# Kernel optimization log

Measured on AMD Instinct MI355X. Metric: run time of the kernel, lower is better.

The kernel has to match this reference:

```python
import jax, jax.numpy as jnp
import numpy as np

B, T_ENC, H_ENC, H_DEC, ATTN = 64, 4096, 512, 512, 256


def setup_inputs() -> dict:
    key = jax.random.key(0)
    k1, k2, k3, k4, k5 = jax.random.split(key, 5)
    decoder_state = jax.random.normal(k1, (B, H_DEC), dtype=jnp.float32)
    encoder_outputs = jax.random.normal(k2, (B, T_ENC, H_ENC), dtype=jnp.float32)
    # nn.Linear(in, out, bias=False) weight has shape (out, in); apply as x @ W.T
    W_enc = jax.random.normal(k3, (ATTN, H_ENC), dtype=jnp.float32) * (1.0 / np.sqrt(H_ENC))
    W_dec = jax.random.normal(k4, (ATTN, H_DEC), dtype=jnp.float32) * (1.0 / np.sqrt(H_DEC))
    v = jax.random.normal(k5, (1, ATTN), dtype=jnp.float32) * (1.0 / np.sqrt(ATTN))
    return {"decoder_state": decoder_state, "encoder_outputs": encoder_outputs,
            "W_enc": W_enc, "W_dec": W_dec, "v": v}


def reference(decoder_state, encoder_outputs, W_enc, W_dec, v):
    # enc_proj: (B, T, A); dec_proj: (B, 1, A)
    enc_proj = jnp.einsum('bte,ae->bta', encoder_outputs, W_enc)
    dec_proj = jnp.einsum('bd,ad->ba', decoder_state, W_dec)[:, None, :]
    energy = jnp.tanh(enc_proj + dec_proj)              # (B, T, A)
    scores = jnp.einsum('bta,a->bt', energy, v[0])      # (B, T)
    attn_weights = jax.nn.softmax(scores, axis=1)       # (B, T)
    context = jnp.einsum('bte,bt->be', encoder_outputs, attn_weights)  # (B, H_enc)
    return context, attn_weights
```

## Files before the change

kernel.cpp:

```cpp
#include <hip/hip_runtime.h>
#include <hip/hip_bf16.h>

#define B 64
#define T_ENC 4096
#define H_ENC 512
#define H_DEC 512
#define ATTN 256

#define BM 128
#define BK 64
#define LDA_A 72
#define NCH_PER_B (T_ENC / BM)
#define NCHUNKS ((B * T_ENC) / BM)

typedef __attribute__((ext_vector_type(8))) short bf16x8;
typedef __attribute__((ext_vector_type(4))) float f32x4;

__device__ __forceinline__ ushort2 cvt2_bf16(float x, float y) {
    __hip_bfloat162 h = __float22bfloat162_rn(make_float2(x, y));
    return *reinterpret_cast<ushort2*>(&h);
}

__device__ __forceinline__ float fast_tanh(float x) {
    float ax = fabsf(x);
    float e = __expf(2.0f * fminf(ax, 15.0f));
    float t = 1.0f - 2.0f / (e + 1.0f);
    return copysignf(t, x);
}

__device__ __forceinline__ void gload_lds16(const void* g, void* l) {
    __builtin_amdgcn_global_load_lds(
        (const __attribute__((address_space(1))) void*)g,
        (__attribute__((address_space(3))) void*)l, 16, 0, 0);
}

__global__ void convw_kernel(const float* __restrict__ W,
                             unsigned short* __restrict__ out) {
    int g = blockIdx.x * 256 + threadIdx.x;
    int j = g & 7;
    int r = (g >> 3) & 255;
    int t = g >> 11;
    int c0 = t * 64 + ((j ^ (r & 7)) << 3);
    const float* src = W + (size_t)r * H_ENC + c0;
    float4 x0 = *(const float4*)(src);
    float4 x1 = *(const float4*)(src + 4);
    ushort2 a0 = cvt2_bf16(x0.x, x0.y);
    ushort2 a1 = cvt2_bf16(x0.z, x0.w);
    ushort2 a2 = cvt2_bf16(x1.x, x1.y);
    ushort2 a3 = cvt2_bf16(x1.z, x1.w);
    ushort4 lo = {a0.x, a0.y, a1.x, a1.y};
    ushort4 hi = {a2.x, a2.y, a3.x, a3.y};
    *(ushort4*)(out + (size_t)g * 8)     = lo;
    *(ushort4*)(out + (size_t)g * 8 + 4) = hi;
}

__global__ void decproj_kernel(const float* __restrict__ dec,
                               const float* __restrict__ Wdec,
                               float* __restrict__ dproj) {
    __shared__ float sdec[H_DEC];
    int b = blockIdx.x;
    int tid = threadIdx.x;
    sdec[tid]       = dec[b * H_DEC + tid];
    sdec[tid + 256] = dec[b * H_DEC + tid + 256];
    __syncthreads();
    const float* wrow = Wdec + (size_t)tid * H_DEC;
    float acc = 0.0f;
#pragma unroll 4
    for (int k = 0; k < H_DEC; k += 4) {
        float4 w4 = *(const float4*)(wrow + k);
        acc += w4.x * sdec[k] + w4.y * sdec[k + 1] + w4.z * sdec[k + 2] + w4.w * sdec[k + 3];
    }
    dproj[b * ATTN + tid] = acc;
}

__global__ __launch_bounds__(256, 2) void fused_kernel(
    const float* __restrict__ enc,
    const unsigned short* __restrict__ wencb,
    const float* __restrict__ dproj,
    const float* __restrict__ v,
    float* __restrict__ scores,
    float* __restrict__ ctxp,
    float* __restrict__ ml)
{
    __shared__ __align__(16) unsigned short Abuf[BM * LDA_A];
    __shared__ __align__(16) unsigned short Bbuf[ATTN * BK];
    __shared__ float sPart[BM * 2];
    __shared__ float sP[BM];
    __shared__ float sW[4];

    const int tid  = threadIdx.x;
    const int wave = tid >> 6;
    const int lane = tid & 63;
    const int quad = lane >> 4;
    const int l16  = lane & 15;
    const int wr   = wave >> 1;
    const int wc   = wave & 1;
    const int swz  = (l16 & 7) << 4;
    const int chunk = blockIdx.x;
    const int m0   = chunk * BM;
    const int b    = chunk >> 5;

    f32x4 acc[4][8];
#pragma unroll
    for (int mi = 0; mi < 4; ++mi)
#pragma unroll
        for (int ni = 0; ni < 8; ++ni) {
            f32x4 z = {0.0f, 0.0f, 0.0f, 0.0f};
            acc[mi][ni] = z;
        }

    const char* wb = (const char*)wencb;
    char* bb = (char*)Bbuf;

    for (int k0 = 0; k0 < H_ENC; k0 += BK) {
        const int t = k0 >> 6;
#pragma unroll
        for (int i = 0; i < 8; ++i) {
            int u = i * 256 + tid;
            gload_lds16(wb + (((size_t)t * 2048 + u) << 4), bb + (u << 4));
        }
#pragma unroll
        for (int rp = 0; rp < 4; ++rp) {
            int idx = rp * 2048 + tid * 8;
            int r = idx >> 6, c = idx & 63;
            const float* p = enc + (size_t)(m0 + r) * H_ENC + k0 + c;
            float4 x0 = *(const float4*)(p);
            float4 x1 = *(const float4*)(p + 4);
            ushort2 a0 = cvt2_bf16(x0.x, x0.y);
            ushort2 a1 = cvt2_bf16(x0.z, x0.w);
            ushort2 a2 = cvt2_bf16(x1.x, x1.y);
            ushort2 a3 = cvt2_bf16(x1.z, x1.w);
            union { bf16x8 v8; unsigned short u[8]; } U;
            U.u[0] = a0.x; U.u[1] = a0.y; U.u[2] = a1.x; U.u[3] = a1.y;
            U.u[4] = a2.x; U.u[5] = a2.y; U.u[6] = a3.x; U.u[7] = a3.y;
            *(bf16x8*)(&Abuf[r * LDA_A + c]) = U.v8;
        }
        __syncthreads();

#pragma unroll
        for (int kk = 0; kk < 2; ++kk) {
            bf16x8 af[4], bfv[8];
            const int ca = kk * 32 + quad * 8;
            const int dc = kk * 64 + quad * 16;
#pragma unroll
            for (int mi = 0; mi < 4; ++mi)
                af[mi] = *(const bf16x8*)(&Abuf[(wr * 64 + mi * 16 + l16) * LDA_A + ca]);
#pragma unroll
            for (int ni = 0; ni < 8; ++ni) {
                int a = wc * 128 + ni * 16 + l16;
                bfv[ni] = *(const bf16x8*)(bb + a * 128 + (dc ^ swz));
            }
#pragma unroll
            for (int mi = 0; mi < 4; ++mi)
#pragma unroll
                for (int ni = 0; ni < 8; ++ni)
                    acc[mi][ni] = __builtin_amdgcn_mfma_f32_16x16x32_bf16(
                        af[mi], bfv[ni], acc[mi][ni], 0, 0, 0);
        }
        __syncthreads();
    }

    float decp[8], vv[8];
#pragma unroll
    for (int ni = 0; ni < 8; ++ni) {
        int a = wc * 128 + ni * 16 + l16;
        decp[ni] = dproj[b * ATTN + a];
        vv[ni]   = v[a];
    }
#pragma unroll
    for (int mi = 0; mi < 4; ++mi) {
#pragma unroll
        for (int r = 0; r < 4; ++r) {
            float sum = 0.0f;
#pragma unroll
            for (int ni = 0; ni < 8; ++ni)
                sum += fast_tanh(acc[mi][ni][r] + decp[ni]) * vv[ni];
            sum += __shfl_xor(sum, 1);
            sum += __shfl_xor(sum, 2);
            sum += __shfl_xor(sum, 4);
            sum += __shfl_xor(sum, 8);
            if (l16 == 0)
                sPart[(wr * 64 + mi * 16 + quad * 4 + r) * 2 + wc] = sum;
        }
    }
    __syncthreads();

    const bool act = tid < BM;
    float s = -INFINITY;
    if (act) {
        s = sPart[tid * 2] + sPart[tid * 2 + 1];
        scores[m0 + tid] = s;
    }
    float m = s;
#pragma unroll
    for (int o = 1; o < 64; o <<= 1) m = fmaxf(m, __shfl_xor(m, o));
    if (act && lane == 0) sW[wave] = m;
    __syncthreads();
    const float M = fmaxf(sW[0], sW[1]);
    float p = act ? __expf(s - M) : 0.0f;
    float l = p;
#pragma unroll
    for (int o = 1; o < 64; o <<= 1) l += __shfl_xor(l, o);
    if (act && lane == 0) sW[2 + wave] = l;
    if (act) sP[tid] = p;
    __syncthreads();
    if (tid == 0) {
        ml[chunk * 2]     = M;
        ml[chunk * 2 + 1] = sW[2] + sW[3];
    }

    int e0 = tid * 2;
    const float* ebase = enc + (size_t)m0 * H_ENC + e0;
    float cx = 0.0f, cy = 0.0f;
#pragma unroll 8
    for (int tt = 0; tt < BM; ++tt) {
        float wt = sP[tt];
        float2 x = *(const float2*)(ebase + (size_t)tt * H_ENC);
        cx += wt * x.x;
        cy += wt * x.y;
    }
    float* cp = ctxp + (size_t)chunk * H_ENC + e0;
    cp[0] = cx;
    cp[1] = cy;
}

__global__ __launch_bounds__(256) void combine_kernel(
    const float* __restrict__ scores,
    const float* __restrict__ ctxp,
    const float* __restrict__ ml,
    float* __restrict__ out)
{
    __shared__ float sc[NCH_PER_B];
    __shared__ float sML[2];
    const int b = blockIdx.x;
    const int tid = threadIdx.x;
    const int nch = NCH_PER_B;

    float m_in = -INFINITY, l_in = 0.0f;
    if (tid < nch) {
        m_in = ml[(b * nch + tid) * 2];
        l_in = ml[(b * nch + tid) * 2 + 1];
    }
    if (tid < 64) {
        float M = m_in;
#pragma unroll
        for (int o = 1; o < 32; o <<= 1) M = fmaxf(M, __shfl_xor(M, o));
        float scale = (tid < nch) ? __expf(m_in - M) : 0.0f;
        float L = l_in * scale;
#pragma unroll
        for (int o = 1; o < 32; o <<= 1) L += __shfl_xor(L, o);
        if (tid < nch) sc[tid] = scale;
        if (tid == 0) { sML[0] = M; sML[1] = L; }
    }
    __syncthreads();
    const float M = sML[0];
    const float invL = 1.0f / sML[1];

    const float* sb = scores + (size_t)b * T_ENC;
    float* attn = out + B * H_ENC + (size_t)b * T_ENC;
#pragma unroll
    for (int i = 0; i < 16; ++i) {
        int t = i * 256 + tid;
        attn[t] = __expf(sb[t] - M) * invL;
    }

    int e0 = tid * 2;
    const float* cp = ctxp + ((size_t)b * nch) * H_ENC + e0;
    float cx = 0.0f, cy = 0.0f;
#pragma unroll 4
    for (int i = 0; i < nch; ++i) {
        float s2 = sc[i];
        float2 x = *(const float2*)(cp + (size_t)i * H_ENC);
        cx += s2 * x.x;
        cy += s2 * x.y;
    }
    out[b * H_ENC + e0]     = cx * invL;
    out[b * H_ENC + e0 + 1] = cy * invL;
}

extern "C" void kernel_launch(void* const* d_in, const int* in_sizes, int n_in,
                              void* d_out, int out_size, void* d_ws, size_t ws_size,
                              hipStream_t stream) {
    const float* dec  = (const float*)d_in[0];
    const float* enc  = (const float*)d_in[1];
    const float* Wenc = (const float*)d_in[2];
    const float* Wdec = (const float*)d_in[3];
    const float* v    = (const float*)d_in[4];
    float* out = (float*)d_out;
    float* ws  = (float*)d_ws;

    float* scores = ws;
    float* dproj  = scores + (size_t)B * T_ENC;
    unsigned short* wencb = (unsigned short*)(dproj + B * ATTN);
    float* ctxp = dproj + B * ATTN + (ATTN * H_ENC) / 2;
    float* ml   = ctxp + (size_t)NCHUNKS * H_ENC;

    hipLaunchKernelGGL(convw_kernel, dim3((ATTN * H_ENC) / (256 * 8)), dim3(256), 0, stream,
                       Wenc, wencb);
    hipLaunchKernelGGL(decproj_kernel, dim3(B), dim3(256), 0, stream, dec, Wdec, dproj);
    hipLaunchKernelGGL(fused_kernel, dim3(NCHUNKS), dim3(256), 0, stream,
                       enc, wencb, dproj, v, scores, ctxp, ml);
    hipLaunchKernelGGL(combine_kernel, dim3(B), dim3(256), 0, stream,
                       scores, ctxp, ml, out);
}
```

Baseline: 788.0 us.

## Double-buffer A tile with register prefetch and read W_enc directly from global

The encoder tile for the next K step is now prefetched into registers while MFMAs run on the current step, and the A tile in LDS is double-buffered. The B operand (bf16 W_enc) is no longer staged into LDS via global_load_lds. Each lane reads its fragments straight from global/L2 in plain row-major layout, and the conversion kernel no longer swizzles. This aims to hide encoder load latency and free LDS, but it adds register pressure from the eight float4 prefetch registers. It also leans on cache hits for the repeated W_enc reads.

```diff
diff --git a/kernel.cpp b/kernel.cpp
--- a/kernel.cpp
+++ b/kernel.cpp
@@ -28,20 +28,10 @@
     return copysignf(t, x);
 }
 
-__device__ __forceinline__ void gload_lds16(const void* g, void* l) {
-    __builtin_amdgcn_global_load_lds(
-        (const __attribute__((address_space(1))) void*)g,
-        (__attribute__((address_space(3))) void*)l, 16, 0, 0);
-}
-
 __global__ void convw_kernel(const float* __restrict__ W,
                              unsigned short* __restrict__ out) {
     int g = blockIdx.x * 256 + threadIdx.x;
-    int j = g & 7;
-    int r = (g >> 3) & 255;
-    int t = g >> 11;
-    int c0 = t * 64 + ((j ^ (r & 7)) << 3);
-    const float* src = W + (size_t)r * H_ENC + c0;
+    const float* src = W + (size_t)g * 8;
     float4 x0 = *(const float4*)(src);
     float4 x1 = *(const float4*)(src + 4);
     ushort2 a0 = cvt2_bf16(x0.x, x0.y);
@@ -82,8 +72,7 @@
     float* __restrict__ ctxp,
     float* __restrict__ ml)
 {
-    __shared__ __align__(16) unsigned short Abuf[BM * LDA_A];
-    __shared__ __align__(16) unsigned short Bbuf[ATTN * BK];
+    __shared__ __align__(16) unsigned short Abuf[2][BM * LDA_A];
     __shared__ float sPart[BM * 2];
     __shared__ float sP[BM];
     __shared__ float sW[4];
@@ -95,7 +84,6 @@
     const int l16  = lane & 15;
     const int wr   = wave >> 1;
     const int wc   = wave & 1;
-    const int swz  = (l16 & 7) << 4;
     const int chunk = blockIdx.x;
     const int m0   = chunk * BM;
     const int b    = chunk >> 5;
@@ -109,23 +97,26 @@
             acc[mi][ni] = z;
         }
 
-    const char* wb = (const char*)wencb;
-    char* bb = (char*)Bbuf;
+    const int sidx = tid * 8;
+    float4 pA[8];
+
+#pragma unroll
+    for (int rp = 0; rp < 4; ++rp) {
+        int idx = rp * 2048 + sidx;
+        int r = idx >> 6, c = idx & 63;
+        const float* p = enc + (size_t)(m0 + r) * H_ENC + c;
+        pA[rp * 2]     = *(const float4*)(p);
+        pA[rp * 2 + 1] = *(const float4*)(p + 4);
+    }
 
     for (int k0 = 0; k0 < H_ENC; k0 += BK) {
-        const int t = k0 >> 6;
-#pragma unroll
-        for (int i = 0; i < 8; ++i) {
-            int u = i * 256 + tid;
-            gload_lds16(wb + (((size_t)t * 2048 + u) << 4), bb + (u << 4));
-        }
+        const int cur = (k0 >> 6) & 1;
 #pragma unroll
         for (int rp = 0; rp < 4; ++rp) {
-            int idx = rp * 2048 + tid * 8;
+            int idx = rp * 2048 + sidx;
             int r = idx >> 6, c = idx & 63;
-            const float* p = enc + (size_t)(m0 + r) * H_ENC + k0 + c;
-            float4 x0 = *(const float4*)(p);
-            float4 x1 = *(const float4*)(p + 4);
+            float4 x0 = pA[rp * 2];
+            float4 x1 = pA[rp * 2 + 1];
             ushort2 a0 = cvt2_bf16(x0.x, x0.y);
             ushort2 a1 = cvt2_bf16(x0.z, x0.w);
             ushort2 a2 = cvt2_bf16(x1.x, x1.y);
@@ -133,22 +124,32 @@
             union { bf16x8 v8; unsigned short u[8]; } U;
             U.u[0] = a0.x; U.u[1] = a0.y; U.u[2] = a1.x; U.u[3] = a1.y;
             U.u[4] = a2.x; U.u[5] = a2.y; U.u[6] = a3.x; U.u[7] = a3.y;
-            *(bf16x8*)(&Abuf[r * LDA_A + c]) = U.v8;
+            *(bf16x8*)(&Abuf[cur][r * LDA_A + c]) = U.v8;
         }
         __syncthreads();
 
+        if (k0 + BK < H_ENC) {
+#pragma unroll
+            for (int rp = 0; rp < 4; ++rp) {
+                int idx = rp * 2048 + sidx;
+                int r = idx >> 6, c = idx & 63;
+                const float* p = enc + (size_t)(m0 + r) * H_ENC + (k0 + BK) + c;
+                pA[rp * 2]     = *(const float4*)(p);
+                pA[rp * 2 + 1] = *(const float4*)(p + 4);
+            }
+        }
+
 #pragma unroll
         for (int kk = 0; kk < 2; ++kk) {
+            const int ca = kk * 32 + quad * 8;
             bf16x8 af[4], bfv[8];
-            const int ca = kk * 32 + quad * 8;
-            const int dc = kk * 64 + quad * 16;
 #pragma unroll
             for (int mi = 0; mi < 4; ++mi)
-                af[mi] = *(const bf16x8*)(&Abuf[(wr * 64 + mi * 16 + l16) * LDA_A + ca]);
+                af[mi] = *(const bf16x8*)(&Abuf[cur][(wr * 64 + mi * 16 + l16) * LDA_A + ca]);
 #pragma unroll
             for (int ni = 0; ni < 8; ++ni) {
                 int a = wc * 128 + ni * 16 + l16;
-                bfv[ni] = *(const bf16x8*)(bb + a * 128 + (dc ^ swz));
+                bfv[ni] = *(const bf16x8*)(wencb + (size_t)a * H_ENC + k0 + ca);
             }
 #pragma unroll
             for (int mi = 0; mi < 4; ++mi)
```

Result: slower. 835.4 us (+6.0%).
